# Performance work log

Hardware: AMD Instinct MI355X
Metric: run time of the kernel (lower is better)

The kernel has to match this reference:

```python
import jax, jax.numpy as jnp
import numpy as np

P_DROP = 0.1

def setup_inputs() -> dict:
    key = jax.random.key(0)
    kq, kk, kv, km = jax.random.split(key, 4)
    B, H, S, D = 2, 16, 2048, 128
    q = jax.random.normal(kq, (B, H, S, D), dtype=jnp.float32)
    k = jax.random.normal(kk, (B, H, S, D), dtype=jnp.float32)
    v = jax.random.normal(kv, (B, H, S, D), dtype=jnp.float32)
    # Deterministic inverted-dropout mask: keep with prob 1-p, scaled by 1/(1-p)
    keep = jax.random.bernoulli(km, 1.0 - P_DROP, (B, H, S, S))
    drop_mask = keep.astype(jnp.float32) / jnp.float32(1.0 - P_DROP)
    return {"q": q, "k": k, "v": v, "drop_mask": drop_mask}

def reference(q, k, v, drop_mask):
    # qk: [B,H,S,S] = q @ k^T (no softmax, per the original module)
    qk = jnp.einsum("bhsd,bhtd->bhst", q, k)
    dropped = qk * drop_mask  # inverted dropout, p=0.1
    out = jnp.einsum("bhst,bhtd->bhsd", dropped, v)
    return out
```

## Files before the change

kernel.cpp:

```cpp
#include <hip/hip_runtime.h>

#define S_LEN 2048
#define D_DIM 128
#define BM 128
#define BK 64
#define NIT (S_LEN / BK)
#define LQ 136
#define LV 72
#define KS_E (BK * LQ)
#define VT_E (D_DIM * LV)
#define BUF_E (KS_E + VT_E)

typedef __attribute__((ext_vector_type(8))) short bf16x8;
typedef __attribute__((ext_vector_type(4))) float f32x4;
typedef __attribute__((ext_vector_type(4))) int i32x4;

__device__ __forceinline__ unsigned rnd16(float x) {
    union { float f; unsigned u; } c; c.f = x;
    return c.u + 0x8000u;
}
__device__ __forceinline__ unsigned pack2(float lo, float hi) {
    return __builtin_amdgcn_perm(rnd16(hi), rnd16(lo), 0x07060302);
}

__global__ __launch_bounds__(256, 2)
void fused_qkmv(const float* __restrict__ q, const float* __restrict__ k,
                const float* __restrict__ v, const float* __restrict__ mask,
                float* __restrict__ out) {
    __shared__ __align__(16) unsigned short smem[2 * BUF_E];
    unsigned short* const Qst = smem;

    const int tid  = threadIdx.x;
    const int lane = tid & 63;
    const int w    = tid >> 6;
    const int l15  = lane & 15;
    const int qd   = lane >> 4;

    const int bh = blockIdx.x >> 4;
    const int s0 = (blockIdx.x & 15) * BM;

    const float* qp = q + (size_t)bh * S_LEN * D_DIM;
    const float* kp = k + (size_t)bh * S_LEN * D_DIM;
    const float* vp = v + (size_t)bh * S_LEN * D_DIM;
    const float* mp = mask + (size_t)bh * S_LEN * S_LEN;
    float*       op = out + (size_t)bh * S_LEN * D_DIM;

    const int rr = tid >> 5, dd = (tid & 31) * 4;
    const int tg = (tid & 15) * 4, dg = (tid >> 4) * 8;

    float4 kf[8];
#pragma unroll
    for (int sw = 0; sw < 8; ++sw)
        kf[sw] = *(const float4*)(kp + (size_t)(sw * 8 + rr) * D_DIM + dd);
    float4 va[4], vb[4];
#pragma unroll
    for (int r = 0; r < 4; ++r) {
        va[r] = *(const float4*)(vp + (size_t)(tg + r) * D_DIM + dg);
        vb[r] = *(const float4*)(vp + (size_t)(tg + r) * D_DIM + dg + 4);
    }
    float4 mreg[4][2];
    {
        const float* mb = mp + (size_t)(s0 + 32 * w + l15) * S_LEN + 4 * qd;
#pragma unroll
        for (int ti = 0; ti < 4; ++ti)
#pragma unroll
            for (int sj = 0; sj < 2; ++sj)
                mreg[ti][sj] = *(const float4*)(mb + (size_t)sj * 16 * S_LEN + ti * 16);
    }
#pragma unroll
    for (int sw = 0; sw < 16; ++sw) {
        const int row = sw * 8 + rr;
        float4 f = *(const float4*)(qp + (size_t)(s0 + row) * D_DIM + dd);
        uint2 wv; wv.x = pack2(f.x, f.y); wv.y = pack2(f.z, f.w);
        *(uint2*)&Qst[row * LQ + dd] = wv;
    }
    __syncthreads();
    bf16x8 qf[2][4];
#pragma unroll
    for (int sj = 0; sj < 2; ++sj)
#pragma unroll
        for (int kc = 0; kc < 4; ++kc)
            qf[sj][kc] = *(const bf16x8*)&Qst[(32 * w + 16 * sj + l15) * LQ + kc * 32 + qd * 8];
    __syncthreads();
#pragma unroll
    for (int sw = 0; sw < 8; ++sw) {
        uint2 wv; wv.x = pack2(kf[sw].x, kf[sw].y); wv.y = pack2(kf[sw].z, kf[sw].w);
        *(uint2*)&smem[(sw * 8 + rr) * LQ + dd] = wv;
    }
#pragma unroll
    for (int i = 0; i < 4; ++i) {
        uint2 wv;
        wv.x = pack2(((const float*)&va[0])[i], ((const float*)&va[1])[i]);
        wv.y = pack2(((const float*)&va[2])[i], ((const float*)&va[3])[i]);
        *(uint2*)&smem[KS_E + (dg + i) * LV + tg] = wv;
        uint2 wv2;
        wv2.x = pack2(((const float*)&vb[0])[i], ((const float*)&vb[1])[i]);
        wv2.y = pack2(((const float*)&vb[2])[i], ((const float*)&vb[3])[i]);
        *(uint2*)&smem[KS_E + (dg + 4 + i) * LV + tg] = wv2;
    }
    __syncthreads();

    f32x4 acc_o[2][8];
#pragma unroll
    for (int i = 0; i < 2; ++i)
#pragma unroll
        for (int j = 0; j < 8; ++j) acc_o[i][j] = (f32x4){0.f, 0.f, 0.f, 0.f};

    const int a0 = ((2 * (qd & 1)) * 16 + l15) * 4;
    const int a1 = a0 + 64;
    const bool hi = (qd >= 2);

    int cur = 0;
    for (int it = 0; it < NIT; ++it) {
        const int nxt = cur ^ 1;
        const int tn = (it + 1) * BK;
        const bool pf = (it + 1 < NIT);
        const unsigned short* Ksc = smem + cur * BUF_E;
        const unsigned short* Vtc = smem + cur * BUF_E + KS_E;
        unsigned short* Ksn = smem + nxt * BUF_E;
        unsigned short* Vtn = smem + nxt * BUF_E + KS_E;

        if (pf) {
#pragma unroll
            for (int sw = 0; sw < 8; ++sw)
                kf[sw] = *(const float4*)(kp + (size_t)(tn + sw * 8 + rr) * D_DIM + dd);
        }

        f32x4 acc_s[4][2];
#pragma unroll
        for (int i = 0; i < 4; ++i)
#pragma unroll
            for (int j = 0; j < 2; ++j) acc_s[i][j] = (f32x4){0.f, 0.f, 0.f, 0.f};
#pragma unroll
        for (int kc = 0; kc < 4; ++kc) {
            const int ko = kc * 32 + qd * 8;
            bf16x8 af[4];
#pragma unroll
            for (int ti = 0; ti < 4; ++ti)
                af[ti] = *(const bf16x8*)&Ksc[(16 * ti + l15) * LQ + ko];
#pragma unroll
            for (int ti = 0; ti < 4; ++ti)
#pragma unroll
                for (int sj = 0; sj < 2; ++sj)
                    acc_s[ti][sj] = __builtin_amdgcn_mfma_f32_16x16x32_bf16(
                        af[ti], qf[sj][kc], acc_s[ti][sj], 0, 0, 0);
        }

        if (pf) {
#pragma unroll
            for (int sw = 0; sw < 8; ++sw) {
                uint2 wv; wv.x = pack2(kf[sw].x, kf[sw].y); wv.y = pack2(kf[sw].z, kf[sw].w);
                *(uint2*)&Ksn[(sw * 8 + rr) * LQ + dd] = wv;
            }
#pragma unroll
            for (int r = 0; r < 4; ++r) {
                va[r] = *(const float4*)(vp + (size_t)(tn + tg + r) * D_DIM + dg);
                vb[r] = *(const float4*)(vp + (size_t)(tn + tg + r) * D_DIM + dg + 4);
            }
        }

        int pu[4][2][2];
#pragma unroll
        for (int ti = 0; ti < 4; ++ti)
#pragma unroll
            for (int sj = 0; sj < 2; ++sj) {
                f32x4 sv = acc_s[ti][sj];
                float4 m = mreg[ti][sj];
                pu[ti][sj][0] = (int)pack2(sv[0] * m.x, sv[1] * m.y);
                pu[ti][sj][1] = (int)pack2(sv[2] * m.z, sv[3] * m.w);
            }

        if (pf) {
            const float* mb = mp + (size_t)(s0 + 32 * w + l15) * S_LEN + tn + 4 * qd;
#pragma unroll
            for (int ti = 0; ti < 4; ++ti)
#pragma unroll
                for (int sj = 0; sj < 2; ++sj)
                    mreg[ti][sj] = *(const float4*)(mb + (size_t)sj * 16 * S_LEN + ti * 16);
        }

#pragma unroll
        for (int kc2 = 0; kc2 < 2; ++kc2) {
            bf16x8 ap[2];
#pragma unroll
            for (int sj = 0; sj < 2; ++sj) {
                const int tA = 2 * kc2, tB = 2 * kc2 + 1;
                int w0a = __builtin_amdgcn_ds_bpermute(a0, pu[tA][sj][0]);
                int w0b = __builtin_amdgcn_ds_bpermute(a0, pu[tB][sj][0]);
                int w1a = __builtin_amdgcn_ds_bpermute(a0, pu[tA][sj][1]);
                int w1b = __builtin_amdgcn_ds_bpermute(a0, pu[tB][sj][1]);
                int w2a = __builtin_amdgcn_ds_bpermute(a1, pu[tA][sj][0]);
                int w2b = __builtin_amdgcn_ds_bpermute(a1, pu[tB][sj][0]);
                int w3a = __builtin_amdgcn_ds_bpermute(a1, pu[tA][sj][1]);
                int w3b = __builtin_amdgcn_ds_bpermute(a1, pu[tB][sj][1]);
                union { i32x4 i; bf16x8 b; } u;
                u.i = (i32x4){hi ? w0b : w0a, hi ? w1b : w1a,
                              hi ? w2b : w2a, hi ? w3b : w3a};
                ap[sj] = u.b;
            }
            const int ko = kc2 * 32 + qd * 8;
#pragma unroll
            for (int dj = 0; dj < 8; ++dj) {
                bf16x8 bv = *(const bf16x8*)&Vtc[(16 * dj + l15) * LV + ko];
#pragma unroll
                for (int si = 0; si < 2; ++si)
                    acc_o[si][dj] = __builtin_amdgcn_mfma_f32_16x16x32_bf16(
                        ap[si], bv, acc_o[si][dj], 0, 0, 0);
            }
        }

        if (pf) {
#pragma unroll
            for (int i = 0; i < 4; ++i) {
                uint2 wv;
                wv.x = pack2(((const float*)&va[0])[i], ((const float*)&va[1])[i]);
                wv.y = pack2(((const float*)&va[2])[i], ((const float*)&va[3])[i]);
                *(uint2*)&Vtn[(dg + i) * LV + tg] = wv;
                uint2 wv2;
                wv2.x = pack2(((const float*)&vb[0])[i], ((const float*)&vb[1])[i]);
                wv2.y = pack2(((const float*)&vb[2])[i], ((const float*)&vb[3])[i]);
                *(uint2*)&Vtn[(dg + 4 + i) * LV + tg] = wv2;
            }
        }

        __syncthreads();
        cur = nxt;
    }

#pragma unroll
    for (int si = 0; si < 2; ++si)
#pragma unroll
        for (int dj = 0; dj < 8; ++dj) {
#pragma unroll
            for (int r = 0; r < 4; ++r) {
                const int srow = s0 + 32 * w + 16 * si + 4 * qd + r;
                op[(size_t)srow * D_DIM + 16 * dj + l15] = acc_o[si][dj][r];
            }
        }
}

extern "C" void kernel_launch(void* const* d_in, const int* in_sizes, int n_in,
                              void* d_out, int out_size, void* d_ws, size_t ws_size,
                              hipStream_t stream) {
    const float* q = (const float*)d_in[0];
    const float* k = (const float*)d_in[1];
    const float* v = (const float*)d_in[2];
    const float* m = (const float*)d_in[3];
    float* out = (float*)d_out;
    fused_qkmv<<<dim3(512), dim3(256), 0, stream>>>(q, k, v, m, out);
}
```

Measured before the change: 807.7 us.

## Pre-convert K/V to swizzled bf16 images and stream them via async global-to-LDS loads

Adds a prep kernel that converts K and V to bf16 once, writing K row-major and V transposed, both XOR-swizzled, into workspace images. The main kernel then fills its double-buffered LDS tiles directly with global_load_lds 16-byte async copies instead of loading fp32 into registers, packing, and storing. Q is packed straight into registers, skipping the LDS staging pass, and the mask prefetch goes to a separate register set. The aim is to cut per-iteration fp32 traffic and conversion work that is repeated by every block sharing a head, and to free registers. The cost is an extra kernel launch plus the workspace write and read round-trip.

```diff
diff --git a/kernel.cpp b/kernel.cpp
--- a/kernel.cpp
+++ b/kernel.cpp
@@ -1,15 +1,11 @@
 #include <hip/hip_runtime.h>
+#include <stdint.h>
 
 #define S_LEN 2048
 #define D_DIM 128
-#define BM 128
 #define BK 64
 #define NIT (S_LEN / BK)
-#define LQ 136
-#define LV 72
-#define KS_E (BK * LQ)
-#define VT_E (D_DIM * LV)
-#define BUF_E (KS_E + VT_E)
+#define KIMG_BYTES (32u * 2048u * 256u)
 
 typedef __attribute__((ext_vector_type(8))) short bf16x8;
 typedef __attribute__((ext_vector_type(4))) float f32x4;
@@ -23,12 +19,60 @@
     return __builtin_amdgcn_perm(rnd16(hi), rnd16(lo), 0x07060302);
 }
 
+__device__ __forceinline__ void async_cp16(const void* g, void* l) {
+    __builtin_amdgcn_global_load_lds(
+        (const __attribute__((address_space(1))) unsigned int*)g,
+        (__attribute__((address_space(3))) unsigned int*)l, 16, 0, 0);
+}
+
+__global__ __launch_bounds__(256)
+void prep(const float* __restrict__ k, const float* __restrict__ v,
+          unsigned char* __restrict__ kimg, unsigned char* __restrict__ vimg) {
+    if (blockIdx.x < 4096) {
+        const unsigned g = blockIdx.x * 256 + threadIdx.x;
+        const int cb = g & 15, t = (g >> 4) & 2047, head = g >> 15;
+        const float* src = k + ((size_t)head * 2048 + t) * 128 + cb * 8;
+        float4 f0 = *(const float4*)src, f1 = *(const float4*)(src + 4);
+        uint4 u;
+        u.x = pack2(f0.x, f0.y); u.y = pack2(f0.z, f0.w);
+        u.z = pack2(f1.x, f1.y); u.w = pack2(f1.z, f1.w);
+        *(uint4*)(kimg + ((size_t)(head * 2048 + t) * 16 + (cb ^ (t & 15))) * 16) = u;
+    } else {
+        const int b = blockIdx.x - 4096;
+        const int head = b >> 5, it = b & 31;
+        const int tid = threadIdx.x;
+        const int tg = (tid & 15) * 4, dg = (tid >> 4) * 8;
+        const float* src = v + (size_t)head * 2048 * 128 + (size_t)(it * 64 + tg) * 128;
+        float4 va[4], vb4[4];
+#pragma unroll
+        for (int r = 0; r < 4; ++r) {
+            va[r]  = *(const float4*)(src + r * 128 + dg);
+            vb4[r] = *(const float4*)(src + r * 128 + dg + 4);
+        }
+        unsigned char* dst = vimg + ((size_t)head * 32 + it) * 16384;
+        const int half = (tg & 4) * 2;
+#pragma unroll
+        for (int i = 0; i < 4; ++i) {
+            const int d = dg + i;
+            uint2 wv;
+            wv.x = pack2(((const float*)&va[0])[i], ((const float*)&va[1])[i]);
+            wv.y = pack2(((const float*)&va[2])[i], ((const float*)&va[3])[i]);
+            *(uint2*)(dst + d * 128 + (((tg >> 3) ^ (d & 7)) * 16) + half) = wv;
+            const int d2 = dg + 4 + i;
+            uint2 w2;
+            w2.x = pack2(((const float*)&vb4[0])[i], ((const float*)&vb4[1])[i]);
+            w2.y = pack2(((const float*)&vb4[2])[i], ((const float*)&vb4[3])[i]);
+            *(uint2*)(dst + d2 * 128 + (((tg >> 3) ^ (d2 & 7)) * 16) + half) = w2;
+        }
+    }
+}
+
 __global__ __launch_bounds__(256, 2)
-void fused_qkmv(const float* __restrict__ q, const float* __restrict__ k,
-                const float* __restrict__ v, const float* __restrict__ mask,
+void fused_main(const float* __restrict__ q, const float* __restrict__ mask,
+                const unsigned char* __restrict__ kimg,
+                const unsigned char* __restrict__ vimg,
                 float* __restrict__ out) {
-    __shared__ __align__(16) unsigned short smem[2 * BUF_E];
-    unsigned short* const Qst = smem;
+    __shared__ __align__(16) unsigned short smem[2 * 16384];
 
     const int tid  = threadIdx.x;
     const int lane = tid & 63;
@@ -37,66 +81,45 @@
     const int qd   = lane >> 4;
 
     const int bh = blockIdx.x >> 4;
-    const int s0 = (blockIdx.x & 15) * BM;
+    const int s0 = (blockIdx.x & 15) * 128;
 
     const float* qp = q + (size_t)bh * S_LEN * D_DIM;
-    const float* kp = k + (size_t)bh * S_LEN * D_DIM;
-    const float* vp = v + (size_t)bh * S_LEN * D_DIM;
     const float* mp = mask + (size_t)bh * S_LEN * S_LEN;
     float*       op = out + (size_t)bh * S_LEN * D_DIM;
-
-    const int rr = tid >> 5, dd = (tid & 31) * 4;
-    const int tg = (tid & 15) * 4, dg = (tid >> 4) * 8;
-
-    float4 kf[8];
-#pragma unroll
-    for (int sw = 0; sw < 8; ++sw)
-        kf[sw] = *(const float4*)(kp + (size_t)(sw * 8 + rr) * D_DIM + dd);
-    float4 va[4], vb[4];
-#pragma unroll
-    for (int r = 0; r < 4; ++r) {
-        va[r] = *(const float4*)(vp + (size_t)(tg + r) * D_DIM + dg);
-        vb[r] = *(const float4*)(vp + (size_t)(tg + r) * D_DIM + dg + 4);
-    }
-    float4 mreg[4][2];
+    const unsigned char* kb = kimg + (size_t)bh * (2048u * 256u);
+    const unsigned char* vb = vimg + (size_t)bh * (32u * 16384u);
+
+    bf16x8 qf[2][4];
+#pragma unroll
+    for (int sj = 0; sj < 2; ++sj)
+#pragma unroll
+        for (int kc = 0; kc < 4; ++kc) {
+            const float* qq = qp + (size_t)(s0 + 32 * w + 16 * sj + l15) * D_DIM
+                            + kc * 32 + qd * 8;
+            float4 f0 = *(const float4*)qq, f1 = *(const float4*)(qq + 4);
+            union { uint4 u; bf16x8 b; } cv;
+            cv.u.x = pack2(f0.x, f0.y); cv.u.y = pack2(f0.z, f0.w);
+            cv.u.z = pack2(f1.x, f1.y); cv.u.w = pack2(f1.z, f1.w);
+            qf[sj][kc] = cv.b;
+        }
+
+    const float* mbase = mp + (size_t)(s0 + 32 * w + l15) * S_LEN + 4 * qd;
+    float4 mcur[4][2], mnxt[4][2];
+#pragma unroll
+    for (int ti = 0; ti < 4; ++ti)
+#pragma unroll
+        for (int sj = 0; sj < 2; ++sj)
+            mcur[ti][sj] = *(const float4*)(mbase + (size_t)(16 * sj) * S_LEN + 16 * ti);
+
     {
-        const float* mb = mp + (size_t)(s0 + 32 * w + l15) * S_LEN + 4 * qd;
-#pragma unroll
-        for (int ti = 0; ti < 4; ++ti)
-#pragma unroll
-            for (int sj = 0; sj < 2; ++sj)
-                mreg[ti][sj] = *(const float4*)(mb + (size_t)sj * 16 * S_LEN + ti * 16);
-    }
-#pragma unroll
-    for (int sw = 0; sw < 16; ++sw) {
-        const int row = sw * 8 + rr;
-        float4 f = *(const float4*)(qp + (size_t)(s0 + row) * D_DIM + dd);
-        uint2 wv; wv.x = pack2(f.x, f.y); wv.y = pack2(f.z, f.w);
-        *(uint2*)&Qst[row * LQ + dd] = wv;
-    }
-    __syncthreads();
-    bf16x8 qf[2][4];
-#pragma unroll
-    for (int sj = 0; sj < 2; ++sj)
-#pragma unroll
-        for (int kc = 0; kc < 4; ++kc)
-            qf[sj][kc] = *(const bf16x8*)&Qst[(32 * w + 16 * sj + l15) * LQ + kc * 32 + qd * 8];
-    __syncthreads();
-#pragma unroll
-    for (int sw = 0; sw < 8; ++sw) {
-        uint2 wv; wv.x = pack2(kf[sw].x, kf[sw].y); wv.y = pack2(kf[sw].z, kf[sw].w);
-        *(uint2*)&smem[(sw * 8 + rr) * LQ + dd] = wv;
-    }
-#pragma unroll
-    for (int i = 0; i < 4; ++i) {
-        uint2 wv;
-        wv.x = pack2(((const float*)&va[0])[i], ((const float*)&va[1])[i]);
-        wv.y = pack2(((const float*)&va[2])[i], ((const float*)&va[3])[i]);
-        *(uint2*)&smem[KS_E + (dg + i) * LV + tg] = wv;
-        uint2 wv2;
-        wv2.x = pack2(((const float*)&vb[0])[i], ((const float*)&vb[1])[i]);
-        wv2.y = pack2(((const float*)&vb[2])[i], ((const float*)&vb[3])[i]);
-        *(uint2*)&smem[KS_E + (dg + 4 + i) * LV + tg] = wv2;
+        unsigned short* lb = smem;
+#pragma unroll
+        for (int s = 0; s < 8; ++s) {
+            const int seg = w + s * 4;
+            const unsigned char* g = (seg < 16) ? (kb + seg * 1024)
+                                                : (vb + (seg - 16) * 1024);
+            async_cp16(g + lane * 16, (void*)(lb + seg * 512 + lane * 8));
+        }
     }
     __syncthreads();
 
@@ -112,18 +135,28 @@
 
     int cur = 0;
     for (int it = 0; it < NIT; ++it) {
+        const bool pf = (it + 1 < NIT);
         const int nxt = cur ^ 1;
-        const int tn = (it + 1) * BK;
-        const bool pf = (it + 1 < NIT);
-        const unsigned short* Ksc = smem + cur * BUF_E;
-        const unsigned short* Vtc = smem + cur * BUF_E + KS_E;
-        unsigned short* Ksn = smem + nxt * BUF_E;
-        unsigned short* Vtn = smem + nxt * BUF_E + KS_E;
+        const unsigned short* Ks = smem + cur * 16384;
+        const unsigned short* Vt = smem + cur * 16384 + 8192;
 
         if (pf) {
-#pragma unroll
-            for (int sw = 0; sw < 8; ++sw)
-                kf[sw] = *(const float4*)(kp + (size_t)(tn + sw * 8 + rr) * D_DIM + dd);
+            const unsigned char* kt = kb + (size_t)(it + 1) * 16384;
+            const unsigned char* vt = vb + (size_t)(it + 1) * 16384;
+            unsigned short* lb = smem + nxt * 16384;
+#pragma unroll
+            for (int s = 0; s < 8; ++s) {
+                const int seg = w + s * 4;
+                const unsigned char* g = (seg < 16) ? (kt + seg * 1024)
+                                                    : (vt + (seg - 16) * 1024);
+                async_cp16(g + lane * 16, (void*)(lb + seg * 512 + lane * 8));
+            }
+            const float* mb = mbase + (size_t)(it + 1) * BK;
+#pragma unroll
+            for (int ti = 0; ti < 4; ++ti)
+#pragma unroll
+                for (int sj = 0; sj < 2; ++sj)
+                    mnxt[ti][sj] = *(const float4*)(mb + (size_t)(16 * sj) * S_LEN + 16 * ti);
         }
 
         f32x4 acc_s[4][2];
@@ -133,11 +166,11 @@
             for (int j = 0; j < 2; ++j) acc_s[i][j] = (f32x4){0.f, 0.f, 0.f, 0.f};
 #pragma unroll
         for (int kc = 0; kc < 4; ++kc) {
-            const int ko = kc * 32 + qd * 8;
             bf16x8 af[4];
 #pragma unroll
             for (int ti = 0; ti < 4; ++ti)
-                af[ti] = *(const bf16x8*)&Ksc[(16 * ti + l15) * LQ + ko];
+                af[ti] = *(const bf16x8*)&Ks[((16 * ti + l15) << 7) +
+                                             (((kc * 4 + qd) ^ l15) << 3)];
 #pragma unroll
             for (int ti = 0; ti < 4; ++ti)
 #pragma unroll
@@ -146,38 +179,16 @@
                         af[ti], qf[sj][kc], acc_s[ti][sj], 0, 0, 0);
         }
 
-        if (pf) {
-#pragma unroll
-            for (int sw = 0; sw < 8; ++sw) {
-                uint2 wv; wv.x = pack2(kf[sw].x, kf[sw].y); wv.y = pack2(kf[sw].z, kf[sw].w);
-                *(uint2*)&Ksn[(sw * 8 + rr) * LQ + dd] = wv;
-            }
-#pragma unroll
-            for (int r = 0; r < 4; ++r) {
-                va[r] = *(const float4*)(vp + (size_t)(tn + tg + r) * D_DIM + dg);
-                vb[r] = *(const float4*)(vp + (size_t)(tn + tg + r) * D_DIM + dg + 4);
-            }
-        }
-
         int pu[4][2][2];
 #pragma unroll
         for (int ti = 0; ti < 4; ++ti)
 #pragma unroll
             for (int sj = 0; sj < 2; ++sj) {
                 f32x4 sv = acc_s[ti][sj];
-                float4 m = mreg[ti][sj];
+                float4 m = mcur[ti][sj];
                 pu[ti][sj][0] = (int)pack2(sv[0] * m.x, sv[1] * m.y);
                 pu[ti][sj][1] = (int)pack2(sv[2] * m.z, sv[3] * m.w);
             }
-
-        if (pf) {
-            const float* mb = mp + (size_t)(s0 + 32 * w + l15) * S_LEN + tn + 4 * qd;
-#pragma unroll
-            for (int ti = 0; ti < 4; ++ti)
-#pragma unroll
-                for (int sj = 0; sj < 2; ++sj)
-                    mreg[ti][sj] = *(const float4*)(mb + (size_t)sj * 16 * S_LEN + ti * 16);
-        }
 
 #pragma unroll
         for (int kc2 = 0; kc2 < 2; ++kc2) {
@@ -198,45 +209,36 @@
                               hi ? w2b : w2a, hi ? w3b : w3a};
                 ap[sj] = u.b;
             }
-            const int ko = kc2 * 32 + qd * 8;
 #pragma unroll
             for (int dj = 0; dj < 8; ++dj) {
-                bf16x8 bv = *(const bf16x8*)&Vtc[(16 * dj + l15) * LV + ko];
-#pragma unroll
-                for (int si = 0; si < 2; ++si)
-                    acc_o[si][dj] = __builtin_amdgcn_mfma_f32_16x16x32_bf16(
-                        ap[si], bv, acc_o[si][dj], 0, 0, 0);
-            }
-        }
-
+                bf16x8 bvv = *(const bf16x8*)&Vt[((16 * dj + l15) << 6) +
+                                                 (((kc2 * 4 + qd) ^ (l15 & 7)) << 3)];
+#pragma unroll
+                for (int sj = 0; sj < 2; ++sj)
+                    acc_o[sj][dj] = __builtin_amdgcn_mfma_f32_16x16x32_bf16(
+                        ap[sj], bvv, acc_o[sj][dj], 0, 0, 0);
+            }
+        }
+
+        __syncthreads();
         if (pf) {
 #pragma unroll
-            for (int i = 0; i < 4; ++i) {
-                uint2 wv;
-                wv.x = pack2(((const float*)&va[0])[i], ((const float*)&va[1])[i]);
-                wv.y = pack2(((const float*)&va[2])[i], ((const float*)&va[3])[i]);
-                *(uint2*)&Vtn[(dg + i) * LV + tg] = wv;
-                uint2 wv2;
-                wv2.x = pack2(((const float*)&vb[0])[i], ((const float*)&vb[1])[i]);
-                wv2.y = pack2(((const float*)&vb[2])[i], ((const float*)&vb[3])[i]);
-                *(uint2*)&Vtn[(dg + 4 + i) * LV + tg] = wv2;
-            }
-        }
-
-        __syncthreads();
+            for (int ti = 0; ti < 4; ++ti)
+#pragma unroll
+                for (int sj = 0; sj < 2; ++sj) mcur[ti][sj] = mnxt[ti][sj];
+        }
         cur = nxt;
     }
 
 #pragma unroll
     for (int si = 0; si < 2; ++si)
 #pragma unroll
-        for (int dj = 0; dj < 8; ++dj) {
+        for (int dj = 0; dj < 8; ++dj)
 #pragma unroll
             for (int r = 0; r < 4; ++r) {
                 const int srow = s0 + 32 * w + 16 * si + 4 * qd + r;
                 op[(size_t)srow * D_DIM + 16 * dj + l15] = acc_o[si][dj][r];
             }
-        }
 }
 
 extern "C" void kernel_launch(void* const* d_in, const int* in_sizes, int n_in,
@@ -246,6 +248,8 @@
     const float* k = (const float*)d_in[1];
     const float* v = (const float*)d_in[2];
     const float* m = (const float*)d_in[3];
-    float* out = (float*)d_out;
-    fused_qkmv<<<dim3(512), dim3(256), 0, stream>>>(q, k, v, m, out);
-}
+    unsigned char* kimg = (unsigned char*)d_ws;
+    unsigned char* vimg = kimg + KIMG_BYTES;
+    prep<<<dim3(5120), dim3(256), 0, stream>>>(k, v, kimg, vimg);
+    fused_main<<<dim3(512), dim3(256), 0, stream>>>(q, m, kimg, vimg, (float*)d_out);
+}
```

Result: no change. 798.8 us (-1.1%).
